# Optimization experiments

Measured on AMD Instinct MI355X. Metric: run time of the kernel, lower is better.

## Reference

```python
import jax, jax.numpy as jnp
import numpy as np

IMAGE_SIZE = 256
DET = int(IMAGE_SIZE * 2 ** 0.5 + 0.5)  # 362 detector bins (diagonal coverage)
US = 4
N_ACQ = 45                     # acquired views: 0,4,...,176 degrees
N_FULL = (N_ACQ - 1) * US + 1  # 177 full (upsampled) views


def setup_inputs() -> dict:
    key = jax.random.key(0)
    k1, k2 = jax.random.split(key)
    x_source = jax.random.normal(k1, (2, 1, IMAGE_SIZE, IMAGE_SIZE), jnp.float32)
    s_target = jax.random.normal(k2, (2, 1, DET, N_ACQ), jnp.float32)
    theta_acq = np.arange(0, 180, 4, dtype=np.float64)  # 45 acquired angles
    segs = [np.linspace(theta_acq[i], theta_acq[i + 1], US + 1)[:-1] for i in range(N_ACQ - 1)]
    theta_full = np.concatenate(segs + [theta_acq[-1:]]).astype(np.float32)  # [177]
    acq_idx = (np.arange(N_ACQ) * US).astype(np.int32)  # positions of acquired angles in theta_full
    return {"x_source": x_source, "s_target": s_target,
            "thetas_deg": jnp.asarray(theta_full), "acq_idx": jnp.asarray(acq_idx)}


def bilinear_gather(img, xs, ys):
    # img: [B,C,H,W]; xs, ys: pixel coords [A,det,det]; zero outside the image.
    H, W = img.shape[-2], img.shape[-1]
    x0 = jnp.floor(xs); y0 = jnp.floor(ys)
    wx = xs - x0; wy = ys - y0
    x0i = x0.astype(jnp.int32); y0i = y0.astype(jnp.int32)

    def get(yi, xi):
        valid = (xi >= 0) & (xi < W) & (yi >= 0) & (yi < H)
        v = img[:, :, jnp.clip(yi, 0, H - 1), jnp.clip(xi, 0, W - 1)]  # [B,C,A,det,det]
        return jnp.where(valid, v, 0.0)

    return (get(y0i, x0i) * (1 - wy) * (1 - wx)
            + get(y0i, x0i + 1) * (1 - wy) * wx
            + get(y0i + 1, x0i) * wy * (1 - wx)
            + get(y0i + 1, x0i + 1) * wy * wx)


def radon(x, thetas_rad, det):
    # Ray-sum projection: sino[theta, t] = sum_s image(t*cos - s*sin, t*sin + s*cos)
    B, C, H, W = x.shape
    t = jnp.arange(det, dtype=x.dtype) - (det - 1) / 2.0  # centered detector/ray coord
    cos = jnp.cos(thetas_rad)[:, None, None]
    sin = jnp.sin(thetas_rad)[:, None, None]
    T = t[None, :, None]; S = t[None, None, :]
    xs = T * cos - S * sin + (W - 1) / 2.0  # [A,det,det]
    ys = T * sin + S * cos + (H - 1) / 2.0
    return bilinear_gather(x, xs, ys).sum(-1)  # [B,C,A,det]


def ramp_filter(size):
    # skimage/pytorch_radon style ramp built from its real-space kernel
    n = np.concatenate([np.arange(1, size // 2 + 1, 2), np.arange(size // 2 - 1, 0, -2)])
    f = np.zeros(size)
    f[0] = 0.25
    f[1::2] = -1.0 / (np.pi * n) ** 2
    return jnp.asarray(2 * np.real(np.fft.fft(f)), dtype=jnp.float32)


def fbp(sino, thetas_rad, image_size):
    # Filtered back-projection. sino: [B,C,det,A]
    B, C, det, A = sino.shape
    pad = max(64, int(2 ** np.ceil(np.log2(2 * det))))
    filt = ramp_filter(pad)  # [pad]
    sp = jnp.pad(sino, ((0, 0), (0, 0), (0, pad - det), (0, 0)))
    sf = jnp.fft.ifft(jnp.fft.fft(sp, axis=2) * filt[None, None, :, None], axis=2).real
    sf = jnp.transpose(sf[:, :, :det, :], (0, 1, 3, 2)).astype(sino.dtype)  # [B,C,A,det]
    g = jnp.arange(image_size, dtype=sino.dtype) - (image_size - 1) / 2.0
    cos = jnp.cos(thetas_rad); sin = jnp.sin(thetas_rad)
    # detector coordinate hit by each pixel, per angle: t = x*cos + y*sin
    t = (cos[:, None, None] * g[None, None, :]
         + sin[:, None, None] * g[None, :, None] + (det - 1) / 2.0)  # [A,H,W]
    t = t.reshape(A, -1)
    t0 = jnp.floor(t)
    w = t - t0
    t0i = t0.astype(jnp.int32)
    aidx = jnp.arange(A)[:, None]

    def samp(ti):
        valid = (ti >= 0) & (ti < det)
        return jnp.where(valid, sf[:, :, aidx, jnp.clip(ti, 0, det - 1)], 0.0)  # [B,C,A,HW]

    v = samp(t0i) * (1 - w) + samp(t0i + 1) * w
    reco = v.sum(2) * (jnp.pi / (2 * A))
    return reco.reshape(B, C, image_size, image_size)


def reference(x_source, s_target, thetas_deg, acq_idx):
    th = thetas_deg * (jnp.pi / 180.0)
    s = radon(x_source, th, DET)          # [B,C,A,det]
    s = jnp.transpose(s, (0, 1, 3, 2))    # [B,C,det,A] -- angle axis last, as in the module
    # masked data-consistency update: acquired columns become (target - predicted)
    s = s.at[..., acq_idx].set(s_target - s[..., acq_idx])
    return fbp(s, th, IMAGE_SIZE)
```

## Files before the change

### kernel.cpp

```cpp
#include <hip/hip_runtime.h>
#include <math.h>

#define IMG   256
#define NFULL 177
#define DETN  362
#define NACQ  45
#define PAD   1024

#define SINO_OFF 0
#define SF_OFF   131072

#define LDSF  5088
#define TTILE 32
#define SEG   64
#define SEGF  48
#define HALF_T 180.5f

__constant__ const int kByOrder[12] = {5, 6, 4, 7, 3, 8, 2, 9, 1, 10, 0, 11};

__global__ __launch_bounds__(256) void radon_kernel(
    const float* __restrict__ x,
    const float* __restrict__ thetas,
    float* __restrict__ sino)
{
    const int blk = blockIdx.x;
    const int b = blk / NFULL;
    const int a = blk - b * NFULL;
    const int T0 = kByOrder[blockIdx.y] * TTILE;
    const int tid = threadIdx.x;
    const int ts = tid & 7;
    const int tt = tid >> 3;
    const int T = T0 + tt;

    __shared__ __align__(16) float tile[LDSF];
    __shared__ int sRange[2];

    const float th = thetas[a] * (float)(M_PI / 180.0);
    const float c = cosf(th);
    const float s = sinf(th);
    const float cx = (IMG - 1) * 0.5f;
    const float cy = (IMG - 1) * 0.5f;
    const float Tc = (float)T - HALF_T;
    const float xbase = Tc * c + cx;
    const float ybase = Tc * s + cy;

    float lo = -1e30f, hi = 1e30f;
    bool empty = (T >= DETN);
    {   const float aa = -s;
        if (aa > 1e-5f)       { lo = fmaxf(lo, (-1.0f - xbase) / aa); hi = fminf(hi, (256.0f - xbase) / aa); }
        else if (aa < -1e-5f) { lo = fmaxf(lo, (256.0f - xbase) / aa); hi = fminf(hi, (-1.0f - xbase) / aa); }
        else if (xbase <= -1.0f || xbase >= 256.0f) empty = true;
    }
    {   const float aa = c;
        if (aa > 1e-5f)       { lo = fmaxf(lo, (-1.0f - ybase) / aa); hi = fminf(hi, (256.0f - ybase) / aa); }
        else if (aa < -1e-5f) { lo = fmaxf(lo, (256.0f - ybase) / aa); hi = fminf(hi, (-1.0f - ybase) / aa); }
        else if (ybase <= -1.0f || ybase >= 256.0f) empty = true;
    }
    lo = fmaxf(lo, -200.0f);
    hi = fminf(hi, 200.0f);
    int Slo = max(0, (int)floorf(lo + HALF_T) - 1);
    int Shi = min(DETN, (int)floorf(hi + HALF_T) + 2);
    if (empty || Shi < Slo) { Slo = 0; Shi = 0; }

    if (tid == 0) { sRange[0] = DETN; sRange[1] = 0; }
    __syncthreads();
    if (Shi > Slo) { atomicMin(&sRange[0], Slo); atomicMax(&sRange[1], Shi); }
    __syncthreads();
    const int SloB = sRange[0], ShiB = sRange[1];

    const float* __restrict__ img = x + b * IMG * IMG;

    const float TcA = (float)T0 - HALF_T;
    const float TcB = (float)(T0 + TTILE - 1) - HALF_T;
    const float xAB_mn = fminf(TcA * c + cx, TcB * c + cx);
    const float xAB_mx = fmaxf(TcA * c + cx, TcB * c + cx);
    const float yAB_mn = fminf(TcA * s + cy, TcB * s + cy);
    const float yAB_mx = fmaxf(TcA * s + cy, TcB * s + cy);

    float val = 0.0f;
    int Sseg = SloB;
    while (Sseg < ShiB) {
        int segLen = SEG;
        int Send, ix0, iy0, w4, h, pitchd;
        for (int attempt = 0; attempt < 2; ++attempt) {
            Send = min(Sseg + segLen, ShiB);
            const float sv0 = (float)Sseg - HALF_T;
            const float sv1 = sv0 + (float)(segLen - 1);
            const float sx0 = sv0 * s, sx1 = sv1 * s;
            const float cy0 = sv0 * c, cy1 = sv1 * c;
            const float xmn = xAB_mn - fmaxf(sx0, sx1);
            const float xmx = xAB_mx - fminf(sx0, sx1);
            const float ymn = yAB_mn + fminf(cy0, cy1);
            const float ymx = yAB_mx + fmaxf(cy0, cy1);
            ix0 = (int)floorf(xmn) - 1;
            iy0 = (int)floorf(ymn) - 1;
            const int w = (int)floorf(xmx) + 3 - ix0;
            h = (int)floorf(ymx) + 3 - iy0;
            const int ix0a = ix0 & ~3;
            const int wal  = (ix0 + w) - ix0a;
            w4 = (wal + 3) >> 2;
            pitchd = w4 << 2;
            if ((pitchd & 7) == 0) pitchd += 4;
            if (pitchd * h <= LDSF) break;
            segLen = SEGF;
        }
        const int ix0a = ix0 & ~3;
        const int total4 = w4 * h;
        const unsigned magic = (1u << 22) / (unsigned)w4 + 1;

        for (int f = tid; f < total4; f += 256) {
            const int r  = (int)(((unsigned)f * magic) >> 22);
            const int c4 = f - r * w4;
            const int gy = iy0 + r;
            const int gx = ix0a + (c4 << 2);
            const int cyc = min(max(gy, 0), IMG - 1);
            const int cxc = min(max(gx, 0), IMG - 4);
            float4 v = *(const float4*)(img + cyc * IMG + cxc);
            const bool ok = ((unsigned)gy < (unsigned)IMG) &
                            ((unsigned)gx <= (unsigned)(IMG - 4));
            if (!ok) v = make_float4(0.f, 0.f, 0.f, 0.f);
            *(float4*)(tile + r * pitchd + (c4 << 2)) = v;
        }
        __syncthreads();

        const float xoff = xbase - (float)ix0a;
        const float yoff = ybase - (float)iy0;
        if (Send - Sseg == SEG) {
            const float s0 = (float)(Sseg + ts) - HALF_T;
            #pragma unroll 4
            for (int u = 0; u < 8; ++u) {
                const float sval = s0 + (float)(8 * u);
                const float xs = fmaf(-sval, s, xoff);
                const float ys = fmaf(sval, c, yoff);
                const float x0f = floorf(xs);
                const float y0f = floorf(ys);
                const float wx = xs - x0f;
                const float wy = ys - y0f;
                const int base = (int)y0f * pitchd + (int)x0f;
                const float v00 = tile[base];
                const float v01 = tile[base + 1];
                const float v10 = tile[base + pitchd];
                const float v11 = tile[base + pitchd + 1];
                const float h0 = fmaf(wx, v01 - v00, v00);
                const float h1 = fmaf(wx, v11 - v10, v10);
                val += fmaf(wy, h1 - h0, h0);
            }
        } else {
            for (int S = Sseg + ts; S < Send; S += 8) {
                const float sval = (float)S - HALF_T;
                const float xs = fmaf(-sval, s, xoff);
                const float ys = fmaf(sval, c, yoff);
                const float x0f = floorf(xs);
                const float y0f = floorf(ys);
                const float wx = xs - x0f;
                const float wy = ys - y0f;
                const int base = (int)y0f * pitchd + (int)x0f;
                const float v00 = tile[base];
                const float v01 = tile[base + 1];
                const float v10 = tile[base + pitchd];
                const float v11 = tile[base + pitchd + 1];
                const float h0 = fmaf(wx, v01 - v00, v00);
                const float h1 = fmaf(wx, v11 - v10, v10);
                val += fmaf(wy, h1 - h0, h0);
            }
        }
        __syncthreads();
        Sseg = Send;
    }

    val += __shfl_xor(val, 1, 8);
    val += __shfl_xor(val, 2, 8);
    val += __shfl_xor(val, 4, 8);
    if (ts == 0 && T < DETN) {
        sino[(b * NFULL + a) * DETN + T] = val;
    }
}

__global__ __launch_bounds__(192) void dc_filter_kernel(
    const float* __restrict__ sino,
    const float* __restrict__ st,
    const int*   __restrict__ acq,
    float* __restrict__ sf)
{
    const int blk = blockIdx.x;
    const int b = blk / NFULL;
    const int a = blk - b * NFULL;
    const int tid = threadIdx.x;

    __shared__ float col[DETN];
    __shared__ float gf[PAD];

    const float SC = (float)(M_PI / (2.0 * NFULL));
    const float c0 = 0.5f * SC;
    for (int n = tid; n < PAD; n += 192) {
        float v = 0.0f;
        if (n & 1) {
            const int d = (n < PAD - n) ? n : (PAD - n);
            const float pd = (float)M_PI * (float)d;
            v = -2.0f / (pd * pd) * SC;
        }
        gf[n] = v;
    }

    int inv = -1;
    for (int i = 0; i < NACQ; ++i) {
        if (acq[i] == a) inv = i;
    }

    for (int m = tid; m < DETN; m += 192) {
        float val = sino[(b * NFULL + a) * DETN + m];
        if (inv >= 0) {
            val = st[(b * DETN + m) * NACQ + inv] - val;
        }
        col[m] = val;
    }
    __syncthreads();

    const int T = blockIdx.y * 181 + tid;
    if (tid < 181) {
        const int m0 = (T + 1) & 1;
        float acc = c0 * col[T];
        #pragma unroll 4
        for (int k = 0; k < 181; ++k) {
            const int m = m0 + 2 * k;
            acc += col[m] * gf[(T - m) & (PAD - 1)];
        }
        sf[(b * NFULL + a) * DETN + T] = acc;
    }
}

__global__ __launch_bounds__(256) void backproject_kernel(
    const float* __restrict__ sf,
    const float* __restrict__ thetas,
    float* __restrict__ out)
{
    __shared__ float cb[2 * NFULL];
    __shared__ float red[256];
    const int tid = threadIdx.x;
    const int lane  = tid & 63;
    const int phase = tid >> 6;
    const int pix = blockIdx.x * 64 + lane;
    const int b = pix >> 16;
    const int y = (pix >> 8) & 255;
    const int xq = pix & 255;
    const float gx = (float)xq - (IMG - 1) * 0.5f;
    const float gy = (float)y  - (IMG - 1) * 0.5f;

    for (int a = tid; a < NFULL; a += 256) {
        float th = thetas[a] * (float)(M_PI / 180.0);
        cb[2 * a]     = cosf(th);
        cb[2 * a + 1] = fmaf(sinf(th), gy, HALF_T);
    }
    __syncthreads();

    const float* __restrict__ sfb = sf + b * NFULL * DETN;

    float acc = 0.0f;
    #pragma unroll 4
    for (int a = phase; a < NFULL; a += 4) {
        const float cs = cb[2 * a];
        const float bs = cb[2 * a + 1];
        const float t = fmaf(cs, gx, bs);
        const float t0f = floorf(t);
        const float w = t - t0f;
        const float* row = sfb + a * DETN + (int)t0f;
        const float v0 = row[0];
        const float v1 = row[1];
        acc += v0 + w * (v1 - v0);
    }
    red[tid] = acc;
    __syncthreads();
    if (tid < 64) {
        out[blockIdx.x * 64 + tid] =
            red[tid] + red[tid + 64] + red[tid + 128] + red[tid + 192];
    }
}

extern "C" void kernel_launch(void* const* d_in, const int* in_sizes, int n_in,
                              void* d_out, int out_size, void* d_ws, size_t ws_size,
                              hipStream_t stream) {
    const float* x      = (const float*)d_in[0];
    const float* st     = (const float*)d_in[1];
    const float* thetas = (const float*)d_in[2];
    const int*   acq    = (const int*)d_in[3];
    float* out  = (float*)d_out;
    float* wsf  = (float*)d_ws;
    float* sino = wsf + SINO_OFF;
    float* sf   = wsf + SF_OFF;

    dim3 gA(2 * NFULL, (DETN + TTILE - 1) / TTILE);
    radon_kernel<<<gA, 256, 0, stream>>>(x, thetas, sino);
    dim3 gB(2 * NFULL, 2);
    dc_filter_kernel<<<gB, 192, 0, stream>>>(sino, st, acq, sf);
    backproject_kernel<<<(2 * IMG * IMG) / 64, 256, 0, stream>>>(sf, thetas, out);
}
```

Baseline: 127.6 us.

## Add prep kernel with padded image, per-angle LDS pitch selection and async global-to-LDS loads

Adds a prep kernel that writes a zero-padded copy of the image into workspace and, for each angle, builds a bank-conflict histogram to choose a fixed LDS tile pitch and segment length. The radon kernel then dispatches to templated cores with compile-time pitch, which removes the runtime magic division and pitch computation. When the workspace is large enough, tiles are filled with global_load_lds direct loads from the padded image and need no bounds masking. This costs an extra kernel launch and a padded-image copy, and it adds code-size and register pressure from the six template instantiations.

```diff
diff --git a/kernel.cpp b/kernel.cpp
--- a/kernel.cpp
+++ b/kernel.cpp
@@ -9,19 +9,190 @@
 
 #define SINO_OFF 0
 #define SF_OFF   131072
-
-#define LDSF  5088
-#define TTILE 32
-#define SEG   64
-#define SEGF  48
+#define SEL_OFF  128160
+#define PIMG_OFF 262144
+#define PIMG_W   264
+#define PIMG_N   (PIMG_W * PIMG_W)
+
+#define TTILE  32
 #define HALF_T 180.5f
+#define TILE_N 5112
 
 __constant__ const int kByOrder[12] = {5, 6, 4, 7, 3, 8, 2, 9, 1, 10, 0, 11};
 
-__global__ __launch_bounds__(256) void radon_kernel(
-    const float* __restrict__ x,
-    const float* __restrict__ thetas,
-    float* __restrict__ sino)
+__device__ __forceinline__ void gload16(const float* g, float* l) {
+    __builtin_amdgcn_global_load_lds(
+        (const __attribute__((address_space(1))) void*)g,
+        (__attribute__((address_space(3))) void*)l, 16, 0, 0);
+}
+
+__global__ __launch_bounds__(256) void prep_kernel(
+    const float* __restrict__ x, const float* __restrict__ thetas,
+    float* __restrict__ pimg, int* __restrict__ sel, int padded)
+{
+    const int tid = threadIdx.x;
+
+    if (padded) {
+        const int i = blockIdx.x * 256 + tid;
+        const int half = PIMG_W * (PIMG_W / 4);
+        if (i < 2 * half) {
+            const int b  = (i >= half) ? 1 : 0;
+            const int j  = i - b * half;
+            const int py = j / (PIMG_W / 4);
+            const int px = (j - py * (PIMG_W / 4)) << 2;
+            float4 v = make_float4(0.f, 0.f, 0.f, 0.f);
+            if (py >= 4 && py < 260 && px >= 4 && px <= 256) {
+                v = *(const float4*)(x + b * IMG * IMG + (py - 4) * IMG + (px - 4));
+            }
+            *(float4*)(pimg + b * PIMG_N + py * PIMG_W + px) = v;
+        }
+    }
+
+    __shared__ int   hist[96];
+    __shared__ float cs[2];
+    const int a = blockIdx.x;
+    if (tid < 96) hist[tid] = 0;
+    if (tid == 0) {
+        const float th = thetas[a] * (float)(M_PI / 180.0);
+        cs[0] = cosf(th); cs[1] = sinf(th);
+    }
+    __syncthreads();
+    const float c = cs[0], s = cs[1];
+    if (tid < 64) {
+        const int tt = tid >> 3, ts = tid & 7;
+        #pragma unroll
+        for (int p = 0; p < 3; ++p) {
+            const float P  = 68.f + 4.f * (float)p;
+            const float dT = s * P + c;
+            const float dS = c * P - s;
+            const int bank = (int)floorf((float)tt * dT + (float)ts * dS + 0.5f) & 31;
+            atomicAdd(&hist[p * 32 + bank], 1);
+        }
+    }
+    __syncthreads();
+    if (tid == 0) {
+        const float ac  = fabsf(c), as = fabsf(s);
+        const float spx = 31.f * ac + 63.f * as;
+        const float spy = 31.f * as + 63.f * ac;
+        const int   hm[3] = {75, 71, 67};
+        int best = 5, bcost = 1 << 30;
+        for (int p = 0; p < 3; ++p) {
+            int m = 0;
+            for (int k = 0; k < 32; ++k) m = max(m, hist[p * 32 + k]);
+            const float Pf = 68.f + 4.f * (float)p;
+            const bool fit64 = (spx <= Pf - 8.05f) && (spy <= (float)hm[p] - 5.05f);
+            if (fit64) { const int cst = 2 * m;     if (cst < bcost) { bcost = cst; best = p; } }
+            {            const int cst = 2 * m + 3; if (cst < bcost) { bcost = cst; best = p + 3; } }
+        }
+        sel[a] = best;
+    }
+}
+
+template<int P, int L>
+__device__ __forceinline__ float radon_core(
+    const float* __restrict__ img,
+    const float* __restrict__ pimgb,
+    float* tile, const int padded,
+    const float c, const float s,
+    const float xbase, const float ybase,
+    const float xAB_mn, const float xAB_mx,
+    const float yAB_mn, const float yAB_mx,
+    const int SloB, const int ShiB, const int tid)
+{
+    constexpr int W4   = P / 4;
+    constexpr int HMAX = TILE_N / P;
+    const int ts   = tid & 7;
+    const int wid  = tid >> 6;
+    const int lane = tid & 63;
+    float val = 0.0f;
+
+    for (int Sseg = SloB; Sseg < ShiB; Sseg += L) {
+        const float sv0 = (float)Sseg - HALF_T;
+        const float sv1 = sv0 + (float)(L - 1);
+        const float xmn = xAB_mn - sv1 * s;
+        const float ya  = sv0 * c, yb = sv1 * c;
+        const float ymn = yAB_mn + fminf(ya, yb);
+        const float ymx = yAB_mx + fmaxf(ya, yb);
+        const int ix0  = (int)floorf(xmn) - 1;
+        const int iy0  = (int)floorf(ymn) - 1;
+        const int ix0a = ix0 & ~3;
+        const int h    = min((int)floorf(ymx) + 3 - iy0, HMAX);
+        const int total4 = W4 * h;
+
+        if (padded) {
+            const int bx = ix0a + 4, by = iy0 + 4;
+            const int nfull = total4 & ~63;
+            for (int f0 = wid * 64; f0 < nfull; f0 += 256) {
+                const int f  = f0 + lane;
+                const int r  = f / W4;
+                const int c4 = f - r * W4;
+                const int px = min(max(bx + (c4 << 2), 0), PIMG_W - 4);
+                const int py = min(max(by + r, 0), PIMG_W - 1);
+                gload16(pimgb + py * PIMG_W + px, tile + (f0 << 2));
+            }
+            const int f = nfull + tid;
+            if (f < total4) {
+                const int r  = f / W4;
+                const int c4 = f - r * W4;
+                const int px = min(max(bx + (c4 << 2), 0), PIMG_W - 4);
+                const int py = min(max(by + r, 0), PIMG_W - 1);
+                *(float4*)(tile + (f << 2)) =
+                    *(const float4*)(pimgb + py * PIMG_W + px);
+            }
+        } else {
+            for (int f = tid; f < total4; f += 256) {
+                const int r  = f / W4;
+                const int c4 = f - r * W4;
+                const int gy = iy0 + r;
+                const int gx = ix0a + (c4 << 2);
+                const int cyc = min(max(gy, 0), IMG - 1);
+                const int cxc = min(max(gx, 0), IMG - 4);
+                float4 v = *(const float4*)(img + cyc * IMG + cxc);
+                const bool ok = ((unsigned)gy < (unsigned)IMG) &
+                                ((unsigned)gx <= (unsigned)(IMG - 4));
+                if (!ok) v = make_float4(0.f, 0.f, 0.f, 0.f);
+                *(float4*)(tile + (f << 2)) = v;
+            }
+        }
+        __syncthreads();
+
+        const float xoff = xbase - (float)ix0a;
+        const float yoff = ybase - (float)iy0;
+        const int Send = min(Sseg + L, ShiB);
+
+        auto samp = [&](float sval) {
+            const float xs  = fmaf(-sval, s, xoff);
+            const float ys  = fmaf(sval, c, yoff);
+            const float x0f = floorf(xs);
+            const float y0f = floorf(ys);
+            const float wx  = xs - x0f;
+            const float wy  = ys - y0f;
+            const int base = (int)fmaf(y0f, (float)P, x0f);
+            const float v00 = tile[base];
+            const float v01 = tile[base + 1];
+            const float v10 = tile[base + P];
+            const float v11 = tile[base + P + 1];
+            const float h0 = fmaf(wx, v01 - v00, v00);
+            const float h1 = fmaf(wx, v11 - v10, v10);
+            val += fmaf(wy, h1 - h0, h0);
+        };
+
+        if (Send - Sseg == L) {
+            const float s0 = (float)(Sseg + ts) - HALF_T;
+            #pragma unroll 4
+            for (int u = 0; u < L / 8; ++u) samp(s0 + (float)(8 * u));
+        } else {
+            for (int S = Sseg + ts; S < Send; S += 8) samp((float)S - HALF_T);
+        }
+        __syncthreads();
+    }
+    return val;
+}
+
+__global__ __launch_bounds__(256, 8) void radon_kernel(
+    const float* __restrict__ x, const float* __restrict__ pimg,
+    const int* __restrict__ sel, const float* __restrict__ thetas,
+    float* __restrict__ sino, int padded)
 {
     const int blk = blockIdx.x;
     const int b = blk / NFULL;
@@ -32,7 +203,7 @@
     const int tt = tid >> 3;
     const int T = T0 + tt;
 
-    __shared__ __align__(16) float tile[LDSF];
+    __shared__ __align__(16) float tile[TILE_N];
     __shared__ int sRange[2];
 
     const float th = thetas[a] * (float)(M_PI / 180.0);
@@ -68,8 +239,6 @@
     __syncthreads();
     const int SloB = sRange[0], ShiB = sRange[1];
 
-    const float* __restrict__ img = x + b * IMG * IMG;
-
     const float TcA = (float)T0 - HALF_T;
     const float TcB = (float)(T0 + TTILE - 1) - HALF_T;
     const float xAB_mn = fminf(TcA * c + cx, TcB * c + cx);
@@ -77,95 +246,24 @@
     const float yAB_mn = fminf(TcA * s + cy, TcB * s + cy);
     const float yAB_mx = fmaxf(TcA * s + cy, TcB * s + cy);
 
-    float val = 0.0f;
-    int Sseg = SloB;
-    while (Sseg < ShiB) {
-        int segLen = SEG;
-        int Send, ix0, iy0, w4, h, pitchd;
-        for (int attempt = 0; attempt < 2; ++attempt) {
-            Send = min(Sseg + segLen, ShiB);
-            const float sv0 = (float)Sseg - HALF_T;
-            const float sv1 = sv0 + (float)(segLen - 1);
-            const float sx0 = sv0 * s, sx1 = sv1 * s;
-            const float cy0 = sv0 * c, cy1 = sv1 * c;
-            const float xmn = xAB_mn - fmaxf(sx0, sx1);
-            const float xmx = xAB_mx - fminf(sx0, sx1);
-            const float ymn = yAB_mn + fminf(cy0, cy1);
-            const float ymx = yAB_mx + fmaxf(cy0, cy1);
-            ix0 = (int)floorf(xmn) - 1;
-            iy0 = (int)floorf(ymn) - 1;
-            const int w = (int)floorf(xmx) + 3 - ix0;
-            h = (int)floorf(ymx) + 3 - iy0;
-            const int ix0a = ix0 & ~3;
-            const int wal  = (ix0 + w) - ix0a;
-            w4 = (wal + 3) >> 2;
-            pitchd = w4 << 2;
-            if ((pitchd & 7) == 0) pitchd += 4;
-            if (pitchd * h <= LDSF) break;
-            segLen = SEGF;
-        }
-        const int ix0a = ix0 & ~3;
-        const int total4 = w4 * h;
-        const unsigned magic = (1u << 22) / (unsigned)w4 + 1;
-
-        for (int f = tid; f < total4; f += 256) {
-            const int r  = (int)(((unsigned)f * magic) >> 22);
-            const int c4 = f - r * w4;
-            const int gy = iy0 + r;
-            const int gx = ix0a + (c4 << 2);
-            const int cyc = min(max(gy, 0), IMG - 1);
-            const int cxc = min(max(gx, 0), IMG - 4);
-            float4 v = *(const float4*)(img + cyc * IMG + cxc);
-            const bool ok = ((unsigned)gy < (unsigned)IMG) &
-                            ((unsigned)gx <= (unsigned)(IMG - 4));
-            if (!ok) v = make_float4(0.f, 0.f, 0.f, 0.f);
-            *(float4*)(tile + r * pitchd + (c4 << 2)) = v;
-        }
-        __syncthreads();
-
-        const float xoff = xbase - (float)ix0a;
-        const float yoff = ybase - (float)iy0;
-        if (Send - Sseg == SEG) {
-            const float s0 = (float)(Sseg + ts) - HALF_T;
-            #pragma unroll 4
-            for (int u = 0; u < 8; ++u) {
-                const float sval = s0 + (float)(8 * u);
-                const float xs = fmaf(-sval, s, xoff);
-                const float ys = fmaf(sval, c, yoff);
-                const float x0f = floorf(xs);
-                const float y0f = floorf(ys);
-                const float wx = xs - x0f;
-                const float wy = ys - y0f;
-                const int base = (int)y0f * pitchd + (int)x0f;
-                const float v00 = tile[base];
-                const float v01 = tile[base + 1];
-                const float v10 = tile[base + pitchd];
-                const float v11 = tile[base + pitchd + 1];
-                const float h0 = fmaf(wx, v01 - v00, v00);
-                const float h1 = fmaf(wx, v11 - v10, v10);
-                val += fmaf(wy, h1 - h0, h0);
-            }
-        } else {
-            for (int S = Sseg + ts; S < Send; S += 8) {
-                const float sval = (float)S - HALF_T;
-                const float xs = fmaf(-sval, s, xoff);
-                const float ys = fmaf(sval, c, yoff);
-                const float x0f = floorf(xs);
-                const float y0f = floorf(ys);
-                const float wx = xs - x0f;
-                const float wy = ys - y0f;
-                const int base = (int)y0f * pitchd + (int)x0f;
-                const float v00 = tile[base];
-                const float v01 = tile[base + 1];
-                const float v10 = tile[base + pitchd];
-                const float v11 = tile[base + pitchd + 1];
-                const float h0 = fmaf(wx, v01 - v00, v00);
-                const float h1 = fmaf(wx, v11 - v10, v10);
-                val += fmaf(wy, h1 - h0, h0);
-            }
-        }
-        __syncthreads();
-        Sseg = Send;
+    const float* __restrict__ img   = x + b * IMG * IMG;
+    const float* __restrict__ pimgb = pimg + b * PIMG_N;
+    const int selv = sel[a];
+
+    float val;
+    switch (selv) {
+    case 0:  val = radon_core<68,64>(img, pimgb, tile, padded, c, s, xbase, ybase,
+                                     xAB_mn, xAB_mx, yAB_mn, yAB_mx, SloB, ShiB, tid); break;
+    case 1:  val = radon_core<72,64>(img, pimgb, tile, padded, c, s, xbase, ybase,
+                                     xAB_mn, xAB_mx, yAB_mn, yAB_mx, SloB, ShiB, tid); break;
+    case 2:  val = radon_core<76,64>(img, pimgb, tile, padded, c, s, xbase, ybase,
+                                     xAB_mn, xAB_mx, yAB_mn, yAB_mx, SloB, ShiB, tid); break;
+    case 3:  val = radon_core<68,48>(img, pimgb, tile, padded, c, s, xbase, ybase,
+                                     xAB_mn, xAB_mx, yAB_mn, yAB_mx, SloB, ShiB, tid); break;
+    case 4:  val = radon_core<72,48>(img, pimgb, tile, padded, c, s, xbase, ybase,
+                                     xAB_mn, xAB_mx, yAB_mn, yAB_mx, SloB, ShiB, tid); break;
+    default: val = radon_core<76,48>(img, pimgb, tile, padded, c, s, xbase, ybase,
+                                     xAB_mn, xAB_mx, yAB_mn, yAB_mx, SloB, ShiB, tid); break;
     }
 
     val += __shfl_xor(val, 1, 8);
@@ -287,9 +385,15 @@
     float* wsf  = (float*)d_ws;
     float* sino = wsf + SINO_OFF;
     float* sf   = wsf + SF_OFF;
-
-    dim3 gA(2 * NFULL, (DETN + TTILE - 1) / TTILE);
-    radon_kernel<<<gA, 256, 0, stream>>>(x, thetas, sino);
+    int*   sel  = (int*)(wsf + SEL_OFF);
+    float* pimg = wsf + PIMG_OFF;
+
+    const size_t need = (size_t)(PIMG_OFF + 2 * PIMG_N) * sizeof(float);
+    const int padded = (ws_size >= need) ? 1 : 0;
+
+    prep_kernel<<<NFULL, 256, 0, stream>>>(x, thetas, pimg, sel, padded);
+    dim3 gA(2 * NFULL, 12);
+    radon_kernel<<<gA, 256, 0, stream>>>(x, pimg, sel, thetas, sino, padded);
     dim3 gB(2 * NFULL, 2);
     dc_filter_kernel<<<gB, 192, 0, stream>>>(sino, st, acq, sf);
     backproject_kernel<<<(2 * IMG * IMG) / 64, 256, 0, stream>>>(sf, thetas, out);
```

Result: no change. 127.6 us (+0.0%).
